# Kernel tuning notes

Hardware: AMD Instinct MI355X
Metric: run time of the kernel (lower is better)

## Reference

```python
import jax, jax.numpy as jnp
import numpy as np

NOISE_SCALE = 1.0  # GumbelDistribution(0.0, noise_scale)
INPUT_NOISE_TEMP = 1.0
EPS = 1e-10


def setup_inputs() -> dict:
    key = jax.random.key(0)
    k1, k2 = jax.random.split(key)
    S, B, N = 16, 128, 16384
    logits = jax.random.normal(k1, (B, N), dtype=jnp.float32)
    uniform_noise = jax.random.uniform(k2, (S, B, N), dtype=jnp.float32,
                                       minval=EPS, maxval=1.0 - EPS)
    return {"logits": logits, "uniform_noise": uniform_noise, "k": 32}


def _topk_mask(perturbed, k):
    # select_from_candidates: hard 0/1 mask of the top-k candidates per row.
    S, B, N = perturbed.shape
    flat = perturbed.reshape(S * B, N)
    _, idx = jax.lax.top_k(flat, k)                      # [S*B, k]
    rows = jnp.arange(S * B)[:, None]
    mask = jnp.zeros_like(flat).at[rows, idx].set(1.0)
    return mask.reshape(S, B, N)


def reference(logits, uniform_noise, k):
    # IMLE forward: replicate logits nb_samples times, add Gumbel noise,
    # then top-k hard selection per sample.
    gumbel = -jnp.log(-jnp.log(uniform_noise)) * NOISE_SCALE  # Gumbel(0, scale)
    perturbed = logits[None, :, :] + INPUT_NOISE_TEMP * gumbel  # [S, B, N]
    mask = _topk_mask(perturbed, k)
    return mask
```

## Files before the change

kernel.cpp:

```cpp
#include <hip/hip_runtime.h>
#include <math.h>

typedef unsigned int uint32;
typedef unsigned long long uint64;

#define NN       16384
#define THREADS  256
#define VPT      16
#define NCOPY    16
#define CAND_CAP 1024

__device__ __forceinline__ uint32 fkey(float p) {
    const uint32 b = __float_as_uint(p);
    return (b & 0x80000000u) ? ~b : (b | 0x80000000u);
}
__device__ __forceinline__ float fkey_dec(uint32 kk) {
    const uint32 b = (kk & 0x80000000u) ? (kk ^ 0x80000000u) : ~kk;
    return __uint_as_float(b);
}

__device__ __forceinline__ float cr_logf(float x)
{
    const uint32 xb = __float_as_uint(x);
    const uint32 ge = (xb >> 22) & 1u;
    const int    e  = (int)(xb >> 23) - 127 + (int)ge;
    const uint32 mb = (xb & 0x7FFFFFu) | 0x3F800000u;
    const float  mh = __uint_as_float(mb - (ge << 23));
    const double md  = (double)mh;
    const double num = md - 1.0;
    const double den = md + 1.0;
    double r = (double)__builtin_amdgcn_rcpf((float)den);
    r = r * fma(-den, r, 2.0);
    r = r * fma(-den, r, 2.0);
    const double s  = num * r;
    const double s2 = s * s;
    double q;
    q = 1.0/23.0;
    q = fma(q, s2, 1.0/21.0);
    q = fma(q, s2, 1.0/19.0);
    q = fma(q, s2, 1.0/17.0);
    q = fma(q, s2, 1.0/15.0);
    q = fma(q, s2, 1.0/13.0);
    q = fma(q, s2, 1.0/11.0);
    q = fma(q, s2, 1.0/9.0);
    q = fma(q, s2, 1.0/7.0);
    q = fma(q, s2, 1.0/5.0);
    q = fma(q, s2, 1.0/3.0);
    const double s3 = s2 * (2.0 * s);
    const double lm = fma(s3, q, 2.0 * s);
    const double ed = (double)e;
    const double LN2_HI = 6.93147180369123816490e-01;
    const double LN2_LO = 1.90821492927058770002e-10;
    return (float)fma(ed, LN2_HI, fma(ed, LN2_LO, lm));
}

__device__ __forceinline__ void select_byte(const int* __restrict__ finalh,
                                            int rem_in, uint32* sh_bin,
                                            int* sh_rem, int lane, int wid)
{
    if (wid == 0) {
        const int lo = 252 - 4 * lane;
        const int s  = finalh[lo] + finalh[lo+1] + finalh[lo+2] + finalh[lo+3];
        int p = s;
        #pragma unroll
        for (int off = 1; off < 64; off <<= 1) {
            const int v = __shfl_up(p, off);
            if (lane >= off) p += v;
        }
        const uint64 bal = __ballot(p >= rem_in);
        const int l0 = __ffsll((long long)bal) - 1;
        if (lane == l0) {
            int acc = p - s;
            int b   = lo + 3;
            for (;;) {
                const int h = finalh[b];
                if (acc + h >= rem_in || b == lo) break;
                acc += h; --b;
            }
            *sh_bin = (uint32)b;
            *sh_rem = rem_in - acc;
        }
    }
}

__global__ __launch_bounds__(THREADS, 4)
void imle_topk_kernel(const float* __restrict__ logits,
                      const float* __restrict__ noise,
                      const int*   __restrict__ kptr,
                      float*       __restrict__ out,
                      int Brows)
{
    __shared__ int    hist[256 * NCOPY];
    __shared__ int    finalh[256];
    __shared__ uint32 sh_bin;
    __shared__ int    sh_rem;
    __shared__ int    cand_cnt;
    __shared__ int    cand_idx[CAND_CAP];
    __shared__ uint32 cand_key[CAND_CAP];

    const int row  = blockIdx.x;
    const int lrow = row % Brows;
    const int tid  = threadIdx.x;
    const int k    = kptr[0];
    const int lane = tid & 63;
    const int wid  = tid >> 6;

    if (tid == 0) cand_cnt = 0;

    const float4* __restrict__ np4 = (const float4*)(noise  + (size_t)row  * NN);
    const float4* __restrict__ lp4 = (const float4*)(logits + (size_t)lrow * NN);
    float4*       __restrict__ op4 = (float4*)(out + (size_t)row * NN);

    uint32 key[VPT][4];
    const float4 zero4 = make_float4(0.f, 0.f, 0.f, 0.f);

    #pragma unroll
    for (int j = 0; j < VPT; ++j) {
        const int v = tid + j * THREADS;
        const float4 u4 = np4[v];
        const float4 l4 = lp4[v];
        const float uu[4] = {u4.x, u4.y, u4.z, u4.w};
        const float ll[4] = {l4.x, l4.y, l4.z, l4.w};
        #pragma unroll
        for (int c = 0; c < 4; ++c) {
            const float u  = uu[c];
            const float d  = u - 1.0f;
            const float t1g = __log2f(u) * 0.69314718056f;
            const float t1w = d * fmaf(d, fmaf(d, fmaf(d, -0.25f, 0.33333334f), -0.5f), 1.0f);
            const float t1 = (fabsf(d) < 0.015625f) ? t1w : t1g;
            const float t2 = __log2f(-t1) * 0.69314718056f;
            const float p  = ll[c] - t2;
            key[j][c] = fkey(p);
        }
        op4[v] = zero4;
    }
    __syncthreads();

    const int copy = tid & (NCOPY - 1);
    #pragma unroll
    for (int i = 0; i < (256 * NCOPY) / THREADS; ++i)
        hist[tid + i * THREADS] = 0;
    __syncthreads();
    #pragma unroll
    for (int j = 0; j < VPT; ++j) {
        #pragma unroll
        for (int c = 0; c < 4; ++c)
            atomicAdd(&hist[((key[j][c] >> 24) * NCOPY) + copy], 1);
    }
    __syncthreads();
    {
        int ssum = 0;
        #pragma unroll
        for (int q = 0; q < NCOPY; ++q)
            ssum += hist[tid * NCOPY + ((q + tid) & (NCOPY - 1))];
        finalh[tid] = ssum;
    }
    __syncthreads();
    select_byte(finalh, k, &sh_bin, &sh_rem, lane, wid);
    __syncthreads();
    const uint32 b3  = sh_bin;
    const int    rem = sh_rem;

    __syncthreads();
    #pragma unroll
    for (int i = 0; i < (256 * NCOPY) / THREADS; ++i)
        hist[tid + i * THREADS] = 0;
    __syncthreads();
    #pragma unroll
    for (int j = 0; j < VPT; ++j) {
        #pragma unroll
        for (int c = 0; c < 4; ++c) {
            const uint32 kk = key[j][c];
            if ((kk >> 24) == b3)
                atomicAdd(&hist[(((kk >> 16) & 255u) * NCOPY) + copy], 1);
        }
    }
    __syncthreads();
    {
        int ssum = 0;
        #pragma unroll
        for (int q = 0; q < NCOPY; ++q)
            ssum += hist[tid * NCOPY + ((q + tid) & (NCOPY - 1))];
        finalh[tid] = ssum;
    }
    __syncthreads();
    select_byte(finalh, rem, &sh_bin, &sh_rem, lane, wid);
    __syncthreads();
    const uint32 b2 = sh_bin;

    const uint32 Lkey  = (b3 << 24) | (b2 << 16);
    const float  Lf    = fkey_dec(Lkey);
    const float  TloF  = Lf - (3e-4f + fabsf(Lf) * 2e-6f);
    const uint32 Tlo   = fkey(TloF);

    #pragma unroll
    for (int j = 0; j < VPT; ++j) {
        const int v = tid + j * THREADS;
        #pragma unroll
        for (int c = 0; c < 4; ++c) {
            if (key[j][c] >= Tlo) {
                const int slot = atomicAdd(&cand_cnt, 1);
                if (slot < CAND_CAP) cand_idx[slot] = 4 * v + c;
            }
        }
    }
    __syncthreads();
    int n = cand_cnt; if (n > CAND_CAP) n = CAND_CAP;

    const float* __restrict__ nrow = noise  + (size_t)row  * NN;
    const float* __restrict__ lrp  = logits + (size_t)lrow * NN;
    for (int t = tid; t < n; t += THREADS) {
        const int   idx = cand_idx[t];
        const float t1  = cr_logf(nrow[idx]);
        const float t2  = cr_logf(-t1);
        cand_key[t] = fkey(lrp[idx] - t2);
    }
    __syncthreads();

    float* __restrict__ orow = out + (size_t)row * NN;
    for (int t = tid; t < n; t += THREADS) {
        const uint32 mk = cand_key[t];
        const int    mi = cand_idx[t];
        int rank = 0;
        for (int j2 = 0; j2 < n; ++j2) {
            const uint32 ok = cand_key[j2];
            rank += (ok > mk || (ok == mk && cand_idx[j2] < mi)) ? 1 : 0;
        }
        if (rank < k) orow[mi] = 1.0f;
    }
}

extern "C" void kernel_launch(void* const* d_in, const int* in_sizes, int n_in,
                              void* d_out, int out_size, void* d_ws, size_t ws_size,
                              hipStream_t stream) {
    const float* logits = (const float*)d_in[0];
    const float* noise  = (const float*)d_in[1];
    const int*   kptr   = (const int*)d_in[2];
    float*       out    = (float*)d_out;

    const int rows  = in_sizes[1] / NN;
    const int Brows = in_sizes[0] / NN;

    imle_topk_kernel<<<rows, THREADS, 0, stream>>>(logits, noise, kptr, out, Brows);
}
```

Baseline: 259.3 us.

## Pack 16-bit radix keys and double block size to raise occupancy

Keeps only the top 16 bits of each per-element sort key, packed two per register, so a thread holds half as many key registers. Block size grows from 256 to 512 threads with 8 vectors per thread, 8 histogram copies, and a higher launch-bounds occupancy target. The candidate threshold becomes a 16-bit key minus two bins instead of a float-based epsilon band, which may admit more candidates and risks overflowing the smaller candidate buffer. Fewer histogram copies also raise shared-memory atomic contention.

```diff
diff --git a/kernel.cpp b/kernel.cpp
--- a/kernel.cpp
+++ b/kernel.cpp
@@ -5,18 +5,14 @@
 typedef unsigned long long uint64;
 
 #define NN       16384
-#define THREADS  256
-#define VPT      16
-#define NCOPY    16
-#define CAND_CAP 1024
+#define THREADS  512
+#define VPT      8
+#define NCOPY    8
+#define CAND_CAP 768
 
 __device__ __forceinline__ uint32 fkey(float p) {
     const uint32 b = __float_as_uint(p);
     return (b & 0x80000000u) ? ~b : (b | 0x80000000u);
-}
-__device__ __forceinline__ float fkey_dec(uint32 kk) {
-    const uint32 b = (kk & 0x80000000u) ? (kk ^ 0x80000000u) : ~kk;
-    return __uint_as_float(b);
 }
 
 __device__ __forceinline__ float cr_logf(float x)
@@ -83,7 +79,7 @@
     }
 }
 
-__global__ __launch_bounds__(THREADS, 4)
+__global__ __launch_bounds__(THREADS, 8)
 void imle_topk_kernel(const float* __restrict__ logits,
                       const float* __restrict__ noise,
                       const int*   __restrict__ kptr,
@@ -111,7 +107,7 @@
     const float4* __restrict__ lp4 = (const float4*)(logits + (size_t)lrow * NN);
     float4*       __restrict__ op4 = (float4*)(out + (size_t)row * NN);
 
-    uint32 key[VPT][4];
+    uint32 pk[VPT][2];
     const float4 zero4 = make_float4(0.f, 0.f, 0.f, 0.f);
 
     #pragma unroll
@@ -121,6 +117,7 @@
         const float4 l4 = lp4[v];
         const float uu[4] = {u4.x, u4.y, u4.z, u4.w};
         const float ll[4] = {l4.x, l4.y, l4.z, l4.w};
+        uint32 k16[4];
         #pragma unroll
         for (int c = 0; c < 4; ++c) {
             const float u  = uu[c];
@@ -130,8 +127,10 @@
             const float t1 = (fabsf(d) < 0.015625f) ? t1w : t1g;
             const float t2 = __log2f(-t1) * 0.69314718056f;
             const float p  = ll[c] - t2;
-            key[j][c] = fkey(p);
-        }
+            k16[c] = fkey(p) >> 16;
+        }
+        pk[j][0] = k16[0] | (k16[1] << 16);
+        pk[j][1] = k16[2] | (k16[3] << 16);
         op4[v] = zero4;
     }
     __syncthreads();
@@ -143,12 +142,14 @@
     __syncthreads();
     #pragma unroll
     for (int j = 0; j < VPT; ++j) {
-        #pragma unroll
-        for (int c = 0; c < 4; ++c)
-            atomicAdd(&hist[((key[j][c] >> 24) * NCOPY) + copy], 1);
-    }
-    __syncthreads();
-    {
+        const uint32 a = pk[j][0], b = pk[j][1];
+        atomicAdd(&hist[((a >>  8) & 255u) * NCOPY + copy], 1);
+        atomicAdd(&hist[((a >> 24)       ) * NCOPY + copy], 1);
+        atomicAdd(&hist[((b >>  8) & 255u) * NCOPY + copy], 1);
+        atomicAdd(&hist[((b >> 24)       ) * NCOPY + copy], 1);
+    }
+    __syncthreads();
+    if (tid < 256) {
         int ssum = 0;
         #pragma unroll
         for (int q = 0; q < NCOPY; ++q)
@@ -169,14 +170,16 @@
     #pragma unroll
     for (int j = 0; j < VPT; ++j) {
         #pragma unroll
-        for (int c = 0; c < 4; ++c) {
-            const uint32 kk = key[j][c];
-            if ((kk >> 24) == b3)
-                atomicAdd(&hist[(((kk >> 16) & 255u) * NCOPY) + copy], 1);
-        }
-    }
-    __syncthreads();
-    {
+        for (int h = 0; h < 2; ++h) {
+            const uint32 w  = pk[j][h];
+            const uint32 ka = w & 0xFFFFu;
+            const uint32 kb = w >> 16;
+            if ((ka >> 8) == b3) atomicAdd(&hist[(ka & 255u) * NCOPY + copy], 1);
+            if ((kb >> 8) == b3) atomicAdd(&hist[(kb & 255u) * NCOPY + copy], 1);
+        }
+    }
+    __syncthreads();
+    if (tid < 256) {
         int ssum = 0;
         #pragma unroll
         for (int q = 0; q < NCOPY; ++q)
@@ -188,19 +191,24 @@
     __syncthreads();
     const uint32 b2 = sh_bin;
 
-    const uint32 Lkey  = (b3 << 24) | (b2 << 16);
-    const float  Lf    = fkey_dec(Lkey);
-    const float  TloF  = Lf - (3e-4f + fabsf(Lf) * 2e-6f);
-    const uint32 Tlo   = fkey(TloF);
+    const uint32 T16   = (b3 << 8) | b2;
+    const uint32 Tlo16 = (T16 >= 2u) ? (T16 - 2u) : 0u;
 
     #pragma unroll
     for (int j = 0; j < VPT; ++j) {
         const int v = tid + j * THREADS;
         #pragma unroll
-        for (int c = 0; c < 4; ++c) {
-            if (key[j][c] >= Tlo) {
+        for (int h = 0; h < 2; ++h) {
+            const uint32 w  = pk[j][h];
+            const uint32 ka = w & 0xFFFFu;
+            const uint32 kb = w >> 16;
+            if (ka >= Tlo16) {
                 const int slot = atomicAdd(&cand_cnt, 1);
-                if (slot < CAND_CAP) cand_idx[slot] = 4 * v + c;
+                if (slot < CAND_CAP) cand_idx[slot] = 4 * v + 2 * h;
+            }
+            if (kb >= Tlo16) {
+                const int slot = atomicAdd(&cand_cnt, 1);
+                if (slot < CAND_CAP) cand_idx[slot] = 4 * v + 2 * h + 1;
             }
         }
     }
```

Measured after the change: 252.0 us. 1.03x faster.
